# Kernel tuning notes

Measured on AMD Instinct MI355X. Metric: run time of the kernel, lower is better.

Reference implementation:

```python
import jax, jax.numpy as jnp
import numpy as np

N = 25600          # total nodes
B = 64             # graphs in batch
NPG = N // B       # nodes per graph (400)
K = 16             # in-degree (regular graph)
E = N * K          # edges
D = 128            # hidden dim = out dim
L = 4              # DGN layers
NUM_ATOM = 128


def _linear_init(key, out_s, in_s):
    lim = 1.0 / np.sqrt(in_s)
    return jax.random.uniform(key, (out_s, in_s), jnp.float32, -lim, lim)


def setup_inputs() -> dict:
    key = jax.random.key(0)
    ks = jax.random.split(key, 16)
    node_feat = jax.random.randint(ks[0], (N,), 0, NUM_ATOM)
    # K-regular in-degree graph, edges intra-graph; dst sorted
    dst = jnp.repeat(jnp.arange(N), K)                       # [E]
    src_local = jax.random.randint(ks[1], (E,), 0, NPG)
    src = (dst // NPG) * NPG + src_local                     # same graph as dst
    eig = jax.random.normal(ks[2], (E, 2), jnp.float32)
    snorm_n = jnp.full((N, 1), 1.0 / np.sqrt(NPG), jnp.float32)
    graph_ids = jnp.arange(N) // NPG
    emb = jax.random.normal(ks[3], (NUM_ATOM, D), jnp.float32) * 0.02
    pre_W = jnp.stack([_linear_init(jax.random.fold_in(ks[4], i), D, 2 * D) for i in range(L)])
    pre_b = jnp.zeros((L, D), jnp.float32)
    post_W = jnp.stack([_linear_init(jax.random.fold_in(ks[5], i), D, 5 * D) for i in range(L)])
    post_b = jnp.zeros((L, D), jnp.float32)
    r_W0 = _linear_init(ks[6], 64, 128); r_b0 = jnp.zeros((64,), jnp.float32)
    r_W1 = _linear_init(ks[7], 32, 64);  r_b1 = jnp.zeros((32,), jnp.float32)
    r_W2 = _linear_init(ks[8], 128, 32); r_b2 = jnp.zeros((128,), jnp.float32)
    return dict(node_feat=node_feat, src=src, dst=dst, eig=eig, snorm_n=snorm_n,
                graph_ids=graph_ids, emb=emb, pre_W=pre_W, pre_b=pre_b,
                post_W=post_W, post_b=post_b, r_W0=r_W0, r_b0=r_b0,
                r_W1=r_W1, r_b1=r_b1, r_W2=r_W2, r_b2=r_b2)


def _dgn_layer(h, src, dst, eig, snorm_n, Wp, bp, Wq, bq):
    n = h.shape[0]
    # pretrans on edges: Linear(cat(h_src, h_dst))  [E, D]
    z2 = jnp.concatenate([h[src], h[dst]], axis=-1)
    e = jnp.einsum('ei,oi->eo', z2, Wp) + bp
    seg_sum = lambda v: jax.ops.segment_sum(v, dst, num_segments=n, indices_are_sorted=True)
    s = seg_sum(e)
    mean = s / K
    mx = jax.ops.segment_max(e, dst, num_segments=n, indices_are_sorted=True)
    # directional aggregator (eig_idx=1)
    w = eig[:, 1]
    denom = seg_sum(jnp.abs(w)) + 1e-8                       # [n]
    ew = w / denom[dst]                                      # [E]
    dir_agg = jnp.abs(seg_sum(e * ew[:, None]) - seg_sum(ew)[:, None] * h)
    agg = jnp.concatenate([h, mean, s, mx, dir_agg], axis=-1)  # [n, 5D]
    hn = jnp.einsum('ni,oi->no', agg, Wq) + bq
    hn = hn * snorm_n           # graph_norm
    hn = jax.nn.relu(hn)
    return h + hn               # residual (in_dim == out_dim)


def reference(node_feat, src, dst, eig, snorm_n, graph_ids, emb,
              pre_W, pre_b, post_W, post_b,
              r_W0, r_b0, r_W1, r_b1, r_W2, r_b2):
    h = emb[node_feat]                                       # AtomEncoder
    for i in range(L):
        h = _dgn_layer(h, src, dst, eig, snorm_n, pre_W[i], pre_b[i], post_W[i], post_b[i])
    # mean_nodes per graph (equal-sized graphs)
    hg = jax.ops.segment_sum(h, graph_ids, num_segments=B, indices_are_sorted=True) / NPG
    y = jax.nn.relu(hg @ r_W0.T + r_b0)
    y = jax.nn.relu(y @ r_W1.T + r_b1)
    return y @ r_W2.T + r_b2                                 # [B, 128]
```

## Files before the change

kernel.cpp:

```cpp
#include <hip/hip_runtime.h>
#include <cstddef>

#define NN 25600
#define BB 64
#define NPG 400
#define KK 16
#define LL 4

typedef _Float16 half_t;
typedef _Float16 h8 __attribute__((ext_vector_type(8)));
typedef _Float16 h4 __attribute__((ext_vector_type(4)));
typedef float f32x4 __attribute__((ext_vector_type(4)));

__global__ __launch_bounds__(256) void prep_k(const float* __restrict__ preW,
                                              const float* __restrict__ preb,
                                              const float* __restrict__ postW,
                                              half_t* __restrict__ WpreH,
                                              half_t* __restrict__ WpreL,
                                              float* __restrict__ bpre,
                                              half_t* __restrict__ WpostH,
                                              half_t* __restrict__ WpostL) {
  int idx = blockIdx.x * 256 + threadIdx.x;
  const int n1 = LL * 256 * 128;
  const int n2 = n1 + LL * 256;
  const int n3 = n2 + LL * 128 * 512;
  if (idx < n1) {
    int l = idx / 32768;
    int r = idx % 32768;
    int o = r / 128, k = r % 128;
    float v = (o < 128) ? preW[(size_t)l * 32768 + (size_t)o * 256 + k]
                        : preW[(size_t)l * 32768 + (size_t)(o - 128) * 256 + 128 + k];
    half_t hi = (half_t)v;
    WpreH[idx] = hi;
    WpreL[idx] = (half_t)(v - (float)hi);
  } else if (idx < n2) {
    int r = idx - n1;
    int l = r / 256, o = r % 256;
    bpre[r] = (o < 128) ? 0.f : preb[l * 128 + (o - 128)];
  } else if (idx < n3) {
    int r = idx - n2;
    int l = r / 65536;
    int q = r % 65536;
    int o = q / 512, kk = q & 511;
    int j = kk >> 7, k = kk & 127;
    const float* base = postW + (size_t)l * 128 * 640 + (size_t)o * 640;
    float v;
    if (j == 0)      v = base[k];
    else if (j == 1) v = base[128 + k] * (1.f / 16.f) + base[256 + k];
    else if (j == 2) v = base[384 + k];
    else             v = base[512 + k];
    half_t hi = (half_t)v;
    WpostH[r] = hi;
    WpostL[r] = (half_t)(v - (float)hi);
  }
}

__global__ __launch_bounds__(256) void embed_k(const int* __restrict__ nf,
                                               const float* __restrict__ emb,
                                               float* __restrict__ hf,
                                               half_t* __restrict__ Hh,
                                               half_t* __restrict__ Hl) {
  int idx = blockIdx.x * 256 + threadIdx.x;
  int n = idx >> 5;
  int d4 = idx & 31;
  int a = nf[n];
  float4 v = *(const float4*)(emb + (size_t)a * 128 + d4 * 4);
  *(float4*)(hf + (size_t)n * 128 + d4 * 4) = v;
  h4 hi, lo;
  const float* vp = &v.x;
#pragma unroll
  for (int j = 0; j < 4; ++j) {
    half_t h = (half_t)vp[j];
    hi[j] = h;
    lo[j] = (half_t)(vp[j] - (float)h);
  }
  *(h4*)(Hh + (size_t)n * 512 + d4 * 4) = hi;
  *(h4*)(Hl + (size_t)n * 512 + d4 * 4) = lo;
}

template <int MODE>
__global__ __launch_bounds__(256) void mfma_gemm_k(const half_t* __restrict__ Ah_g,
                                                   const half_t* __restrict__ Al_g,
                                                   const half_t* __restrict__ Wh_g,
                                                   const half_t* __restrict__ Wl_g,
                                                   int Kt,
                                                   const float* __restrict__ bias,
                                                   float* __restrict__ outF, int ldo,
                                                   half_t* __restrict__ Oh,
                                                   half_t* __restrict__ Ol,
                                                   const float* __restrict__ snorm) {
  __shared__ half_t Ahs[64][40];
  __shared__ half_t Als[64][40];
  __shared__ half_t Bhs[128][40];
  __shared__ half_t Bls[128][40];
  const int tid = threadIdx.x;
  const int r0 = blockIdx.x * 64;
  const int cb = blockIdx.y * 128;
  const int wid = tid >> 6, lane = tid & 63;
  const int wm = wid >> 1, wn = wid & 1;
  const int lr = lane & 15, lk = (lane >> 4) * 8;
  const int arow = tid >> 2, akp = (tid & 3) * 8;
  const int bcol = tid >> 1, bkp = (tid & 1) * 16;
  const int nk = Kt >> 5;
  f32x4 acc[2][4] = {};

  for (int kc = 0; kc < nk; ++kc) {
    const int k0 = kc * 32;
    {
      const size_t g = (size_t)(r0 + arow) * 512 + k0 + akp;
      *(h8*)&Ahs[arow][akp] = *(const h8*)(Ah_g + g);
      *(h8*)&Als[arow][akp] = *(const h8*)(Al_g + g);
    }
    {
      const size_t g = (size_t)(cb + bcol) * Kt + k0 + bkp;
      *(h8*)&Bhs[bcol][bkp] = *(const h8*)(Wh_g + g);
      *(h8*)&Bhs[bcol][bkp + 8] = *(const h8*)(Wh_g + g + 8);
      *(h8*)&Bls[bcol][bkp] = *(const h8*)(Wl_g + g);
      *(h8*)&Bls[bcol][bkp + 8] = *(const h8*)(Wl_g + g + 8);
    }
    __syncthreads();
    h8 af[2][2], bf[4][2];
#pragma unroll
    for (int mi = 0; mi < 2; ++mi) {
      const int r = wm * 32 + mi * 16 + lr;
      af[mi][0] = *(const h8*)&Ahs[r][lk];
      af[mi][1] = *(const h8*)&Als[r][lk];
    }
#pragma unroll
    for (int nj = 0; nj < 4; ++nj) {
      const int c = wn * 64 + nj * 16 + lr;
      bf[nj][0] = *(const h8*)&Bhs[c][lk];
      bf[nj][1] = *(const h8*)&Bls[c][lk];
    }
#pragma unroll
    for (int mi = 0; mi < 2; ++mi)
#pragma unroll
      for (int nj = 0; nj < 4; ++nj) {
        acc[mi][nj] = __builtin_amdgcn_mfma_f32_16x16x32_f16(af[mi][0], bf[nj][0], acc[mi][nj], 0, 0, 0);
        acc[mi][nj] = __builtin_amdgcn_mfma_f32_16x16x32_f16(af[mi][0], bf[nj][1], acc[mi][nj], 0, 0, 0);
        acc[mi][nj] = __builtin_amdgcn_mfma_f32_16x16x32_f16(af[mi][1], bf[nj][0], acc[mi][nj], 0, 0, 0);
      }
    __syncthreads();
  }
#pragma unroll
  for (int mi = 0; mi < 2; ++mi) {
    const int rowb = r0 + wm * 32 + mi * 16 + (lane >> 4) * 4;
#pragma unroll
    for (int nj = 0; nj < 4; ++nj) {
      const int col = cb + wn * 64 + nj * 16 + lr;
      const float bv = bias[col];
#pragma unroll
      for (int q = 0; q < 4; ++q) {
        const int r = rowb + q;
        float a = acc[mi][nj][q] + bv;
        if (MODE == 0) {
          outF[(size_t)r * ldo + col] = a;
        } else {
          a *= snorm[r];
          a = fmaxf(a, 0.f);
          const float hn = outF[(size_t)r * ldo + col] + a;
          outF[(size_t)r * ldo + col] = hn;
          const half_t hi = (half_t)hn;
          Oh[(size_t)r * 512 + col] = hi;
          Ol[(size_t)r * 512 + col] = (half_t)(hn - (float)hi);
        }
      }
    }
  }
}

__global__ __launch_bounds__(256) void edge_agg_k(const float* __restrict__ pre,
                                                  const float* __restrict__ h,
                                                  const int* __restrict__ src,
                                                  const float* __restrict__ eig,
                                                  half_t* __restrict__ Oh,
                                                  half_t* __restrict__ Ol) {
  const int wave = threadIdx.x >> 6;
  const int lane = threadIdx.x & 63;
  const int n = blockIdx.x * 4 + wave;
  const int ebase = n * KK;
  float wv[KK];
  int sv[KK];
  float denom = 0.f;
#pragma unroll
  for (int e = 0; e < KK; ++e) {
    wv[e] = eig[(size_t)(ebase + e) * 2 + 1];
    sv[e] = src[ebase + e];
    denom += fabsf(wv[e]);
  }
  denom += 1e-8f;
  const float inv = 1.f / denom;
  float sum_ew = 0.f;
#pragma unroll
  for (int e = 0; e < KK; ++e) {
    wv[e] *= inv;
    sum_ew += wv[e];
  }
  float sA0 = 0.f, sA1 = 0.f, wA0 = 0.f, wA1 = 0.f;
  float mA0 = -3.402823466e+38f, mA1 = -3.402823466e+38f;
#pragma unroll
  for (int e = 0; e < KK; ++e) {
    const float* ap = pre + (size_t)sv[e] * 256;
    const float a0 = ap[lane];
    const float a1 = ap[64 + lane];
    sA0 += a0;
    sA1 += a1;
    wA0 = fmaf(wv[e], a0, wA0);
    wA1 = fmaf(wv[e], a1, wA1);
    mA0 = fmaxf(mA0, a0);
    mA1 = fmaxf(mA1, a1);
  }
  const float b0 = pre[(size_t)n * 256 + 128 + lane];
  const float b1 = pre[(size_t)n * 256 + 192 + lane];
  const float h0 = h[(size_t)n * 128 + lane];
  const float h1 = h[(size_t)n * 128 + 64 + lane];
  const size_t base = (size_t)n * 512;
  auto wr = [&](size_t off, float v) {
    const half_t hi = (half_t)v;
    Oh[off] = hi;
    Ol[off] = (half_t)(v - (float)hi);
  };
  wr(base + 128 + lane, sA0 + 16.f * b0);
  wr(base + 192 + lane, sA1 + 16.f * b1);
  wr(base + 256 + lane, mA0 + b0);
  wr(base + 320 + lane, mA1 + b1);
  wr(base + 384 + lane, fabsf(wA0 + sum_ew * (b0 - h0)));
  wr(base + 448 + lane, fabsf(wA1 + sum_ew * (b1 - h1)));
}

__global__ __launch_bounds__(256) void reduce_mlp_k(const float* __restrict__ h,
                                                    const float* __restrict__ W0, const float* __restrict__ b0,
                                                    const float* __restrict__ W1, const float* __restrict__ b1,
                                                    const float* __restrict__ W2, const float* __restrict__ b2,
                                                    float* __restrict__ out) {
  __shared__ float hgs[128];
  __shared__ float red[128];
  __shared__ float y0s[64];
  __shared__ float y1s[32];
  __shared__ float wb[64 * 130];
  const int g = blockIdx.x;
  const int t = threadIdx.x;
  {
    const int d = t & 127, hf = t >> 7;
    const float* p = h + ((size_t)g * NPG + (size_t)hf * 200) * 128 + d;
    float acc = 0.f;
    for (int i = 0; i < 200; ++i) acc += p[(size_t)i * 128];
    if (hf) red[d] = acc;
    __syncthreads();
    if (!hf) hgs[d] = (acc + red[d]) * (1.f / (float)NPG);
  }
  __syncthreads();
  for (int idx = t; idx < 64 * 128; idx += 256) {
    wb[(idx >> 7) * 130 + (idx & 127)] = W0[idx];
  }
  __syncthreads();
  if (t < 64) {
    float a = b0[t];
    const float* w = &wb[t * 130];
    for (int k = 0; k < 128; ++k) a = fmaf(hgs[k], w[k], a);
    y0s[t] = fmaxf(a, 0.f);
  }
  __syncthreads();
  for (int idx = t; idx < 32 * 64; idx += 256) {
    wb[(idx >> 6) * 66 + (idx & 63)] = W1[idx];
  }
  __syncthreads();
  if (t < 32) {
    float a = b1[t];
    const float* w = &wb[t * 66];
    for (int k = 0; k < 64; ++k) a = fmaf(y0s[k], w[k], a);
    y1s[t] = fmaxf(a, 0.f);
  }
  __syncthreads();
  for (int idx = t; idx < 128 * 32; idx += 256) {
    wb[(idx >> 5) * 34 + (idx & 31)] = W2[idx];
  }
  __syncthreads();
  if (t < 128) {
    float a = b2[t];
    const float* w = &wb[t * 34];
    for (int k = 0; k < 32; ++k) a = fmaf(y1s[k], w[k], a);
    out[(size_t)g * 128 + t] = a;
  }
}

extern "C" void kernel_launch(void* const* d_in, const int* in_sizes, int n_in,
                              void* d_out, int out_size, void* d_ws, size_t ws_size,
                              hipStream_t stream) {
  const int* node_feat = (const int*)d_in[0];
  const int* src = (const int*)d_in[1];
  const float* eig = (const float*)d_in[3];
  const float* snorm = (const float*)d_in[4];
  const float* emb = (const float*)d_in[6];
  const float* preW = (const float*)d_in[7];
  const float* preb = (const float*)d_in[8];
  const float* postW = (const float*)d_in[9];
  const float* postb = (const float*)d_in[10];
  const float* rW0 = (const float*)d_in[11];
  const float* rb0 = (const float*)d_in[12];
  const float* rW1 = (const float*)d_in[13];
  const float* rb1 = (const float*)d_in[14];
  const float* rW2 = (const float*)d_in[15];
  const float* rb2 = (const float*)d_in[16];
  float* out = (float*)d_out;

  half_t* Hh = (half_t*)d_ws;
  half_t* Hl = Hh + (size_t)NN * 512;
  float* Hf = (float*)(Hl + (size_t)NN * 512);
  float* pre = Hf + (size_t)NN * 128;
  half_t* WpreH = (half_t*)(pre + (size_t)NN * 256);
  half_t* WpreL = WpreH + (size_t)LL * 256 * 128;
  half_t* WpostH = WpreL + (size_t)LL * 256 * 128;
  half_t* WpostL = WpostH + (size_t)LL * 128 * 512;
  float* bpre = (float*)(WpostL + (size_t)LL * 128 * 512);

  prep_k<<<1540, 256, 0, stream>>>(preW, preb, postW, WpreH, WpreL, bpre, WpostH, WpostL);
  embed_k<<<(NN * 32) / 256, 256, 0, stream>>>(node_feat, emb, Hf, Hh, Hl);

  for (int l = 0; l < LL; ++l) {
    mfma_gemm_k<0><<<dim3(NN / 64, 2), 256, 0, stream>>>(
        Hh, Hl, WpreH + (size_t)l * 32768, WpreL + (size_t)l * 32768, 128,
        bpre + (size_t)l * 256, pre, 256, nullptr, nullptr, nullptr);
    edge_agg_k<<<NN / 4, 256, 0, stream>>>(pre, Hf, src, eig, Hh, Hl);
    mfma_gemm_k<1><<<dim3(NN / 64, 1), 256, 0, stream>>>(
        Hh, Hl, WpostH + (size_t)l * 65536, WpostL + (size_t)l * 65536, 512,
        postb + (size_t)l * 128, Hf, 128, Hh, Hl, snorm);
  }

  reduce_mlp_k<<<BB, 256, 0, stream>>>(Hf, rW0, rb0, rW1, rb1, rW2, rb2, out);
}
```

Baseline: 299.1 us.

## Fuse edge aggregation into post-transform GEMM via LDS-staged aggregates

Merges the edge aggregation kernel and the post-transform GEMM into one kernel. Each block computes sum, max and directional aggregates for 32 nodes and stores them as fp16 hi/lo pairs in shared memory. The GEMM then reads them from there, and reads its weight fragments directly from global memory. This removes the round trip through the 512-wide global activation buffer, which also shrinks the Hh/Hl buffers to 128 columns. The cost is reloading post weights from L2 per block with small per-wave tiles, and serial per-wave aggregation over 8 nodes.

Measured after the change: 443.0 us. 1.48x slower.

```diff
diff --git a/kernel.cpp b/kernel.cpp
--- a/kernel.cpp
+++ b/kernel.cpp
@@ -74,21 +74,16 @@
     hi[j] = h;
     lo[j] = (half_t)(vp[j] - (float)h);
   }
-  *(h4*)(Hh + (size_t)n * 512 + d4 * 4) = hi;
-  *(h4*)(Hl + (size_t)n * 512 + d4 * 4) = lo;
-}
-
-template <int MODE>
-__global__ __launch_bounds__(256) void mfma_gemm_k(const half_t* __restrict__ Ah_g,
-                                                   const half_t* __restrict__ Al_g,
-                                                   const half_t* __restrict__ Wh_g,
-                                                   const half_t* __restrict__ Wl_g,
-                                                   int Kt,
-                                                   const float* __restrict__ bias,
-                                                   float* __restrict__ outF, int ldo,
-                                                   half_t* __restrict__ Oh,
-                                                   half_t* __restrict__ Ol,
-                                                   const float* __restrict__ snorm) {
+  *(h4*)(Hh + (size_t)n * 128 + d4 * 4) = hi;
+  *(h4*)(Hl + (size_t)n * 128 + d4 * 4) = lo;
+}
+
+__global__ __launch_bounds__(256) void pre_gemm_k(const half_t* __restrict__ Ah_g,
+                                                  const half_t* __restrict__ Al_g,
+                                                  const half_t* __restrict__ Wh_g,
+                                                  const half_t* __restrict__ Wl_g,
+                                                  const float* __restrict__ bias,
+                                                  float* __restrict__ outF) {
   __shared__ half_t Ahs[64][40];
   __shared__ half_t Als[64][40];
   __shared__ half_t Bhs[128][40];
@@ -101,18 +96,18 @@
   const int lr = lane & 15, lk = (lane >> 4) * 8;
   const int arow = tid >> 2, akp = (tid & 3) * 8;
   const int bcol = tid >> 1, bkp = (tid & 1) * 16;
-  const int nk = Kt >> 5;
   f32x4 acc[2][4] = {};
 
-  for (int kc = 0; kc < nk; ++kc) {
+#pragma unroll
+  for (int kc = 0; kc < 4; ++kc) {
     const int k0 = kc * 32;
     {
-      const size_t g = (size_t)(r0 + arow) * 512 + k0 + akp;
+      const size_t g = (size_t)(r0 + arow) * 128 + k0 + akp;
       *(h8*)&Ahs[arow][akp] = *(const h8*)(Ah_g + g);
       *(h8*)&Als[arow][akp] = *(const h8*)(Al_g + g);
     }
     {
-      const size_t g = (size_t)(cb + bcol) * Kt + k0 + bkp;
+      const size_t g = (size_t)(cb + bcol) * 128 + k0 + bkp;
       *(h8*)&Bhs[bcol][bkp] = *(const h8*)(Wh_g + g);
       *(h8*)&Bhs[bcol][bkp + 8] = *(const h8*)(Wh_g + g + 8);
       *(h8*)&Bls[bcol][bkp] = *(const h8*)(Wl_g + g);
@@ -151,81 +146,144 @@
       const float bv = bias[col];
 #pragma unroll
       for (int q = 0; q < 4; ++q) {
-        const int r = rowb + q;
-        float a = acc[mi][nj][q] + bv;
-        if (MODE == 0) {
-          outF[(size_t)r * ldo + col] = a;
-        } else {
-          a *= snorm[r];
-          a = fmaxf(a, 0.f);
-          const float hn = outF[(size_t)r * ldo + col] + a;
-          outF[(size_t)r * ldo + col] = hn;
-          const half_t hi = (half_t)hn;
-          Oh[(size_t)r * 512 + col] = hi;
-          Ol[(size_t)r * 512 + col] = (half_t)(hn - (float)hi);
-        }
+        outF[(size_t)(rowb + q) * 256 + col] = acc[mi][nj][q] + bv;
       }
     }
   }
 }
 
-__global__ __launch_bounds__(256) void edge_agg_k(const float* __restrict__ pre,
-                                                  const float* __restrict__ h,
+__global__ __launch_bounds__(256) void agg_post_k(const float* __restrict__ pre,
                                                   const int* __restrict__ src,
                                                   const float* __restrict__ eig,
+                                                  const half_t* __restrict__ Hh,
+                                                  const half_t* __restrict__ Hl,
+                                                  const half_t* __restrict__ Wh,
+                                                  const half_t* __restrict__ Wl,
+                                                  const float* __restrict__ bias,
+                                                  const float* __restrict__ snorm,
+                                                  float* __restrict__ Hf,
                                                   half_t* __restrict__ Oh,
                                                   half_t* __restrict__ Ol) {
-  const int wave = threadIdx.x >> 6;
-  const int lane = threadIdx.x & 63;
-  const int n = blockIdx.x * 4 + wave;
-  const int ebase = n * KK;
-  float wv[KK];
-  int sv[KK];
-  float denom = 0.f;
-#pragma unroll
-  for (int e = 0; e < KK; ++e) {
-    wv[e] = eig[(size_t)(ebase + e) * 2 + 1];
-    sv[e] = src[ebase + e];
-    denom += fabsf(wv[e]);
-  }
-  denom += 1e-8f;
-  const float inv = 1.f / denom;
-  float sum_ew = 0.f;
-#pragma unroll
-  for (int e = 0; e < KK; ++e) {
-    wv[e] *= inv;
-    sum_ew += wv[e];
-  }
-  float sA0 = 0.f, sA1 = 0.f, wA0 = 0.f, wA1 = 0.f;
-  float mA0 = -3.402823466e+38f, mA1 = -3.402823466e+38f;
-#pragma unroll
-  for (int e = 0; e < KK; ++e) {
-    const float* ap = pre + (size_t)sv[e] * 256;
-    const float a0 = ap[lane];
-    const float a1 = ap[64 + lane];
-    sA0 += a0;
-    sA1 += a1;
-    wA0 = fmaf(wv[e], a0, wA0);
-    wA1 = fmaf(wv[e], a1, wA1);
-    mA0 = fmaxf(mA0, a0);
-    mA1 = fmaxf(mA1, a1);
-  }
-  const float b0 = pre[(size_t)n * 256 + 128 + lane];
-  const float b1 = pre[(size_t)n * 256 + 192 + lane];
-  const float h0 = h[(size_t)n * 128 + lane];
-  const float h1 = h[(size_t)n * 128 + 64 + lane];
-  const size_t base = (size_t)n * 512;
-  auto wr = [&](size_t off, float v) {
-    const half_t hi = (half_t)v;
-    Oh[off] = hi;
-    Ol[off] = (half_t)(v - (float)hi);
-  };
-  wr(base + 128 + lane, sA0 + 16.f * b0);
-  wr(base + 192 + lane, sA1 + 16.f * b1);
-  wr(base + 256 + lane, mA0 + b0);
-  wr(base + 320 + lane, mA1 + b1);
-  wr(base + 384 + lane, fabsf(wA0 + sum_ew * (b0 - h0)));
-  wr(base + 448 + lane, fabsf(wA1 + sum_ew * (b1 - h1)));
+  __shared__ half_t Ah[32][392];
+  __shared__ half_t Al[32][392];
+  const int tid = threadIdx.x;
+  const int r0 = blockIdx.x * 32;
+  const int wid = tid >> 6, lane = tid & 63;
+  const int wm = wid >> 1, wn = wid & 1;
+  const int lr = lane & 15, lk = (lane >> 4) * 8;
+
+  for (int i = 0; i < 8; ++i) {
+    const int lrow = wid * 8 + i;
+    const int n = r0 + lrow;
+    const int ebase = n * KK;
+    float wv[KK];
+    int sv[KK];
+    float denom = 0.f;
+#pragma unroll
+    for (int e = 0; e < KK; ++e) {
+      wv[e] = eig[(size_t)(ebase + e) * 2 + 1];
+      sv[e] = src[ebase + e];
+      denom += fabsf(wv[e]);
+    }
+    denom += 1e-8f;
+    const float inv = 1.f / denom;
+    float sum_ew = 0.f;
+#pragma unroll
+    for (int e = 0; e < KK; ++e) {
+      wv[e] *= inv;
+      sum_ew += wv[e];
+    }
+    float sA0 = 0.f, sA1 = 0.f, wA0 = 0.f, wA1 = 0.f;
+    float mA0 = -3.402823466e+38f, mA1 = -3.402823466e+38f;
+#pragma unroll
+    for (int e = 0; e < KK; ++e) {
+      const float* ap = pre + (size_t)sv[e] * 256;
+      const float a0 = ap[lane];
+      const float a1 = ap[64 + lane];
+      sA0 += a0;
+      sA1 += a1;
+      wA0 = fmaf(wv[e], a0, wA0);
+      wA1 = fmaf(wv[e], a1, wA1);
+      mA0 = fmaxf(mA0, a0);
+      mA1 = fmaxf(mA1, a1);
+    }
+    const float b0 = pre[(size_t)n * 256 + 128 + lane];
+    const float b1 = pre[(size_t)n * 256 + 192 + lane];
+    const float h0 = Hf[(size_t)n * 128 + lane];
+    const float h1 = Hf[(size_t)n * 128 + 64 + lane];
+    const int d0 = lane, d1 = lane + 64;
+    auto wr = [&](int kcol, float v) {
+      const half_t hi = (half_t)v;
+      Ah[lrow][kcol] = hi;
+      Al[lrow][kcol] = (half_t)(v - (float)hi);
+    };
+    wr(d0, sA0 + 16.f * b0);
+    wr(d1, sA1 + 16.f * b1);
+    wr(128 + d0, mA0 + b0);
+    wr(128 + d1, mA1 + b1);
+    wr(256 + d0, fabsf(wA0 + sum_ew * (b0 - h0)));
+    wr(256 + d1, fabsf(wA1 + sum_ew * (b1 - h1)));
+  }
+
+  const int frow = r0 + wm * 16 + lr;
+  h8 afh[4][2];
+#pragma unroll
+  for (int hc = 0; hc < 4; ++hc) {
+    afh[hc][0] = *(const h8*)(Hh + (size_t)frow * 128 + hc * 32 + lk);
+    afh[hc][1] = *(const h8*)(Hl + (size_t)frow * 128 + hc * 32 + lk);
+  }
+
+  __syncthreads();
+
+  f32x4 acc[4] = {};
+#pragma unroll
+  for (int ck = 0; ck < 12; ++ck) {
+    const int row = wm * 16 + lr;
+    const h8 a0 = *(const h8*)&Ah[row][ck * 32 + lk];
+    const h8 a1 = *(const h8*)&Al[row][ck * 32 + lk];
+    const int k0 = 128 + ck * 32;
+#pragma unroll
+    for (int nj = 0; nj < 4; ++nj) {
+      const int c = wn * 64 + nj * 16 + lr;
+      const h8 b0v = *(const h8*)(Wh + (size_t)c * 512 + k0 + lk);
+      const h8 b1v = *(const h8*)(Wl + (size_t)c * 512 + k0 + lk);
+      acc[nj] = __builtin_amdgcn_mfma_f32_16x16x32_f16(a0, b0v, acc[nj], 0, 0, 0);
+      acc[nj] = __builtin_amdgcn_mfma_f32_16x16x32_f16(a0, b1v, acc[nj], 0, 0, 0);
+      acc[nj] = __builtin_amdgcn_mfma_f32_16x16x32_f16(a1, b0v, acc[nj], 0, 0, 0);
+    }
+  }
+#pragma unroll
+  for (int hc = 0; hc < 4; ++hc) {
+    const int k0 = hc * 32;
+#pragma unroll
+    for (int nj = 0; nj < 4; ++nj) {
+      const int c = wn * 64 + nj * 16 + lr;
+      const h8 b0v = *(const h8*)(Wh + (size_t)c * 512 + k0 + lk);
+      const h8 b1v = *(const h8*)(Wl + (size_t)c * 512 + k0 + lk);
+      acc[nj] = __builtin_amdgcn_mfma_f32_16x16x32_f16(afh[hc][0], b0v, acc[nj], 0, 0, 0);
+      acc[nj] = __builtin_amdgcn_mfma_f32_16x16x32_f16(afh[hc][0], b1v, acc[nj], 0, 0, 0);
+      acc[nj] = __builtin_amdgcn_mfma_f32_16x16x32_f16(afh[hc][1], b0v, acc[nj], 0, 0, 0);
+    }
+  }
+
+  const int rowb = r0 + wm * 16 + (lane >> 4) * 4;
+#pragma unroll
+  for (int nj = 0; nj < 4; ++nj) {
+    const int col = wn * 64 + nj * 16 + lr;
+    const float bv = bias[col];
+#pragma unroll
+    for (int q = 0; q < 4; ++q) {
+      const int r = rowb + q;
+      float a = acc[nj][q] + bv;
+      a *= snorm[r];
+      a = fmaxf(a, 0.f);
+      const float hn = Hf[(size_t)r * 128 + col] + a;
+      Hf[(size_t)r * 128 + col] = hn;
+      const half_t hi = (half_t)hn;
+      Oh[(size_t)r * 128 + col] = hi;
+      Ol[(size_t)r * 128 + col] = (half_t)(hn - (float)hi);
+    }
+  }
 }
 
 __global__ __launch_bounds__(256) void reduce_mlp_k(const float* __restrict__ h,
@@ -305,26 +363,25 @@
   float* out = (float*)d_out;
 
   half_t* Hh = (half_t*)d_ws;
-  half_t* Hl = Hh + (size_t)NN * 512;
-  float* Hf = (float*)(Hl + (size_t)NN * 512);
+  half_t* Hl = Hh + (size_t)NN * 128;
+  float* Hf = (float*)(Hl + (size_t)NN * 128);
   float* pre = Hf + (size_t)NN * 128;
   half_t* WpreH = (half_t*)(pre + (size_t)NN * 256);
-  half_t* WpreL = WpreH + (size_t)LL * 256 * 128;
-  half_t* WpostH = WpreL + (size_t)LL * 256 * 128;
-  half_t* WpostL = WpostH + (size_t)LL * 128 * 512;
-  float* bpre = (float*)(WpostL + (size_t)LL * 128 * 512);
+  half_t* WpreL = WpreH + (size_t)LL * 32768;
+  half_t* WpostH = WpreL + (size_t)LL * 32768;
+  half_t* WpostL = WpostH + (size_t)LL * 65536;
+  float* bpre = (float*)(WpostL + (size_t)LL * 65536);
 
   prep_k<<<1540, 256, 0, stream>>>(preW, preb, postW, WpreH, WpreL, bpre, WpostH, WpostL);
   embed_k<<<(NN * 32) / 256, 256, 0, stream>>>(node_feat, emb, Hf, Hh, Hl);
 
   for (int l = 0; l < LL; ++l) {
-    mfma_gemm_k<0><<<dim3(NN / 64, 2), 256, 0, stream>>>(
-        Hh, Hl, WpreH + (size_t)l * 32768, WpreL + (size_t)l * 32768, 128,
-        bpre + (size_t)l * 256, pre, 256, nullptr, nullptr, nullptr);
-    edge_agg_k<<<NN / 4, 256, 0, stream>>>(pre, Hf, src, eig, Hh, Hl);
-    mfma_gemm_k<1><<<dim3(NN / 64, 1), 256, 0, stream>>>(
-        Hh, Hl, WpostH + (size_t)l * 65536, WpostL + (size_t)l * 65536, 512,
-        postb + (size_t)l * 128, Hf, 128, Hh, Hl, snorm);
+    pre_gemm_k<<<dim3(NN / 64, 2), 256, 0, stream>>>(
+        Hh, Hl, WpreH + (size_t)l * 32768, WpreL + (size_t)l * 32768,
+        bpre + (size_t)l * 256, pre);
+    agg_post_k<<<NN / 32, 256, 0, stream>>>(
+        pre, src, eig, Hh, Hl, WpostH + (size_t)l * 65536, WpostL + (size_t)l * 65536,
+        postb + (size_t)l * 128, snorm, Hf, Hh, Hl);
   }
 
   reduce_mlp_k<<<BB, 256, 0, stream>>>(Hf, rW0, rb0, rW1, rb1, rW2, rb2, out);
```
